# Performance work log

Hardware: AMD Instinct MI355X
Metric: run time of the kernel (lower is better)

## Reference

```python
import jax, jax.numpy as jnp
import numpy as np

H = W = 512      # image spatial dims
C = 3            # channels
K = 32           # kernel size
S = 4            # stride
P = 10           # padding
THRESH = 0.5     # squared-L2 distance threshold
N_PATCH = (H + 2 * P - K) // S + 1  # 126 patches per dim
D = C * K * K    # 3072 patch feature dim


def setup_inputs() -> dict:
    key = jax.random.key(0)
    k1, k2, k3, k4 = jax.random.split(key, 4)
    image = jax.random.uniform(k1, (H, W, C), dtype=jnp.float32)
    mem = jax.random.normal(k2, (4096, D), dtype=jnp.float32)
    mem2 = jax.random.normal(k3, (4096, D), dtype=jnp.float32)
    mapping = jax.random.randint(k4, (4096,), 0, 4096, dtype=jnp.int64)
    return {"image": image, "mem": mem, "mem2": mem2, "mapping": mapping}


def _unfold(img_chw):
    # torch.nn.functional.unfold: -> [L, C*K*K] with feature order (c, kh, kw)
    padded = jnp.pad(img_chw, ((0, 0), (P, P), (P, P)))
    r = (jnp.arange(N_PATCH) * S)[:, None] + jnp.arange(K)[None, :]  # [nH, K]
    c = (jnp.arange(N_PATCH) * S)[:, None] + jnp.arange(K)[None, :]  # [nW, K]
    # patches: [C, nH, nW, K, K]
    patches = padded[:, r[:, None, :, None], c[None, :, None, :]]
    patches = patches.transpose(1, 2, 0, 3, 4)  # [nH, nW, C, K, K]
    return patches.reshape(N_PATCH * N_PATCH, D)


def _fold(patches_ld):
    # inverse of _unfold: scatter-add overlapping patches, crop padding
    p5 = patches_ld.reshape(N_PATCH, N_PATCH, C, K, K)
    r = (jnp.arange(N_PATCH) * S)[:, None] + jnp.arange(K)[None, :]
    c = (jnp.arange(N_PATCH) * S)[:, None] + jnp.arange(K)[None, :]
    canvas = jnp.zeros((C, H + 2 * P, W + 2 * P), dtype=patches_ld.dtype)
    ci = jnp.arange(C)[None, None, :, None, None]
    ri = r[:, None, None, :, None]
    cci = c[None, :, None, None, :]
    canvas = canvas.at[ci, ri, cci].add(p5)
    return canvas[:, P:P + H, P:P + W]  # [C, H, W]


def reference(image, mem, mem2, mapping):
    img_chw = image.transpose(2, 0, 1)            # [C, H, W]
    u = _unfold(img_chw)                           # [L, D]
    # brute-force squared-L2 1-NN against mem bank (FAISS IndexFlatL2)
    d2 = (jnp.sum(u * u, axis=1, keepdims=True)
          - 2.0 * (u @ mem.T)
          + jnp.sum(mem * mem, axis=1)[None, :])   # [L, N]
    dmin = jnp.min(d2, axis=1)                     # [L]
    idx = jnp.argmin(d2, axis=1)                   # [L]
    # counter-based pattern lookup: mem id -> mem2 pattern id -> reconstruct
    recon = mem2[mapping[idx]]                     # [L, D]
    out_p = jnp.where(dmin[:, None] >= THRESH, u, recon)
    folded = _fold(out_p)                          # [C, H, W]
    out = folded / jnp.max(folded)
    return out.transpose(1, 2, 0)                  # [H, W, C]
```

## Files before the change

kernel.cpp:

```cpp
#include <hip/hip_runtime.h>
#include <stdint.h>

#define HH 512
#define WW 512
#define CC 3
#define KK 32
#define SS 4
#define PP 10
#define NPATCH 126
#define NP2 (NPATCH * NPATCH)
#define DD 3072
#define NMEM 4096
#define THRESHV 0.5f

#define OFF_NORMS  0
#define OFF_PNORM  4096
#define OFF_MODCNT 20480
#define OFF_PMAXA  36864

__device__ inline float wave_max(float v) {
    for (int off = 32; off; off >>= 1) v = fmaxf(v, __shfl_xor(v, off, 64));
    return v;
}
__device__ inline float wave_min(float v) {
    for (int off = 32; off; off >>= 1) v = fminf(v, __shfl_xor(v, off, 64));
    return v;
}
__device__ inline float wave_sum(float v) {
    for (int off = 32; off; off >>= 1) v += __shfl_xor(v, off, 64);
    return v;
}

__device__ inline int cov1(int v) {
    int pv = v + PP;
    int a = pv - (KK - 1);
    int imin = (a <= 0) ? 0 : ((a + SS - 1) >> 2);
    int imax = pv >> 2;
    if (imax > NPATCH - 1) imax = NPATCH - 1;
    return imax - imin + 1;
}

__global__ void fused_main(const float* __restrict__ mem,
                           const float* __restrict__ img,
                           float* __restrict__ norms,
                           float* __restrict__ pnorm,
                           float* __restrict__ pmaxA,
                           float* __restrict__ out) {
    __shared__ float cs[WW];
    __shared__ float smx[4];
    int b = blockIdx.x, tid = threadIdx.x;
    int lane = tid & 63, w = tid >> 6;

    if (b >= 1024) {
        int py = b - 1024;
        if (py >= NPATCH) return;
        int y0 = py * SS - PP;
        float s0 = 0.f, s1 = 0.f;
        int x0c = tid, x1c = tid + 256;
#pragma unroll
        for (int ky = 0; ky < KK; ++ky) {
            int y = y0 + ky;
            if (y >= 0 && y < HH) {
                const float* row = img + (size_t)y * WW * CC;
                const float* p0 = row + x0c * CC;
                const float* p1 = row + x1c * CC;
                s0 += p0[0] * p0[0] + p0[1] * p0[1] + p0[2] * p0[2];
                s1 += p1[0] * p1[0] + p1[1] * p1[1] + p1[2] * p1[2];
            }
        }
        cs[x0c] = s0;
        cs[x1c] = s1;
        __syncthreads();
        if (tid < NPATCH) {
            int x0 = tid * SS - PP;
            float t = 0.f;
#pragma unroll
            for (int kx = 0; kx < KK; ++kx) {
                int xx = x0 + kx;
                if (xx >= 0 && xx < WW) t += cs[xx];
            }
            pnorm[py * NPATCH + tid] = t;
        }
        return;
    }

    float m = -INFINITY;
    if (tid < 192) {
        int f = b * 192 + tid;
        float4 v = ((const float4*)img)[f];
        float r[4] = {v.x, v.y, v.z, v.w};
        int e = f * 4;
#pragma unroll
        for (int k = 0; k < 4; ++k) {
            int px = (e + k) / 3;
            int y = px >> 9, x = px & 511;
            float cv = (float)(cov1(y) * cov1(x));
            r[k] *= cv;
            m = fmaxf(m, r[k]);
        }
        float4 o; o.x = r[0]; o.y = r[1]; o.z = r[2]; o.w = r[3];
        ((float4*)out)[f] = o;
    }

    int row = b * 4 + w;
    const float4* rp = (const float4*)(mem + (size_t)row * DD);
    float4 v[12];
#pragma unroll
    for (int i = 0; i < 12; ++i) v[i] = rp[lane + (i << 6)];
    float s0 = 0.f, s1 = 0.f, s2 = 0.f, s3 = 0.f;
#pragma unroll
    for (int i = 0; i < 12; ++i) {
        s0 += v[i].x * v[i].x; s1 += v[i].y * v[i].y;
        s2 += v[i].z * v[i].z; s3 += v[i].w * v[i].w;
    }
    float s = wave_sum((s0 + s1) + (s2 + s3));
    if (lane == 0) norms[row] = s;

    m = wave_max(m);
    if (lane == 0) smx[w] = m;
    __syncthreads();
    if (tid == 0)
        pmaxA[b] = fmaxf(fmaxf(smx[0], smx[1]), fmaxf(smx[2], smx[3]));
}

__global__ void cert_fix(const float* __restrict__ img,
                         const float* __restrict__ mem,
                         const float* __restrict__ mem2,
                         const int* __restrict__ mapping,
                         const float* __restrict__ norms,
                         const float* __restrict__ pnorm,
                         float* __restrict__ out,
                         uint32_t* __restrict__ modcnt) {
    __shared__ float rmn[4], rmx[4];
    __shared__ float s_mn, s_mx;
    __shared__ float smin[256];
    __shared__ int   sarg[256];
    __shared__ uint32_t s_cnt;
    __shared__ uint32_t s_list[256];
    __shared__ int   s_mod;
    int tid = threadIdx.x, lane = tid & 63, w = tid >> 6;
    if (tid == 0) { s_mod = 0; s_cnt = 0; }

    float mn = INFINITY, mx = -INFINITY;
#pragma unroll
    for (int k = 0; k < 16; ++k) {
        float v = norms[tid + (k << 8)];
        mn = fminf(mn, v); mx = fmaxf(mx, v);
    }
    mn = wave_min(mn); mx = wave_max(mx);
    if (lane == 0) { rmn[w] = mn; rmx[w] = mx; }
    __syncthreads();
    if (tid == 0) {
        s_mn = sqrtf(fminf(fminf(rmn[0], rmn[1]), fminf(rmn[2], rmn[3])));
        s_mx = sqrtf(fmaxf(fmaxf(rmx[0], rmx[1]), fmaxf(rmx[2], rmx[3])));
    }
    __syncthreads();
    float lo = s_mn, hi = s_mx;

    int per = (NP2 + gridDim.x - 1) / gridDim.x;
    int p0 = blockIdx.x * per;
    int p1 = p0 + per; if (p1 > NP2) p1 = NP2;
    for (int p = p0 + tid; p < p1; p += 256) {
        float un = sqrtf(pnorm[p]);
        float gap = 0.f;
        if (un <= lo) gap = lo - un;
        else if (un >= hi) gap = un - hi;
        if (gap * gap < THRESHV) {
            uint32_t pos = atomicAdd(&s_cnt, 1u);
            s_list[pos] = (uint32_t)p;
        }
    }
    __syncthreads();
    uint32_t nf = s_cnt;

    for (uint32_t e = 0; e < nf; ++e) {
        int p = (int)s_list[e];
        int pi = p / NPATCH, pj = p % NPATCH;
        int y0 = pi * SS - PP, x0 = pj * SS - PP;
        float best = INFINITY; int barg = NMEM;
        for (int j = tid; j < NMEM; j += 256) {
            const float* mr = mem + (size_t)j * DD;
            float sacc = 0.f;
            for (int d = 0; d < DD; ++d) {
                int c = d >> 10, rem = d & 1023, ky = rem >> 5, kx = rem & 31;
                int y = y0 + ky, x = x0 + kx;
                float u = (y >= 0 && y < HH && x >= 0 && x < WW)
                              ? img[((size_t)y * WW + x) * CC + c] : 0.f;
                float dif = u - mr[d];
                sacc += dif * dif;
            }
            if (sacc < best) { best = sacc; barg = j; }
        }
        smin[tid] = best; sarg[tid] = barg;
        __syncthreads();
        for (int stride = 128; stride; stride >>= 1) {
            if (tid < stride) {
                float s2 = smin[tid + stride];
                int   a2 = sarg[tid + stride];
                if (s2 < smin[tid] || (s2 == smin[tid] && a2 < sarg[tid])) {
                    smin[tid] = s2; sarg[tid] = a2;
                }
            }
            __syncthreads();
        }
        float dmin = smin[0]; int arg = sarg[0];
        if (dmin < THRESHV) {
            const float* rec = mem2 + (size_t)mapping[arg] * DD;
            for (int d = tid; d < DD; d += 256) {
                int c = d >> 10, rem = d & 1023, ky = rem >> 5, kx = rem & 31;
                int y = y0 + ky, x = x0 + kx;
                if (y >= 0 && y < HH && x >= 0 && x < WW) {
                    float u = img[((size_t)y * WW + x) * CC + c];
                    atomicAdd(&out[((size_t)y * WW + x) * CC + c],
                              rec[d] - u);
                }
            }
            if (tid == 0) s_mod++;
        }
        __syncthreads();
    }
    if (tid == 0) modcnt[blockIdx.x] = (uint32_t)s_mod;
}

__global__ void normalize_k(const uint32_t* __restrict__ modcnt,
                            const float* __restrict__ pmaxA,
                            float* __restrict__ out) {
    __shared__ int s_need;
    __shared__ float red[4];
    __shared__ float s_inv;
    int tid = threadIdx.x, lane = tid & 63, w = tid >> 6;
    if (w == 0) {
        int c = (int)modcnt[lane];
        for (int off = 32; off; off >>= 1) c += __shfl_xor(c, off, 64);
        if (lane == 0) s_need = c;
    }
    __syncthreads();
    float m = -INFINITY;
    if (s_need == 0) {
#pragma unroll
        for (int k = 0; k < 4; ++k)
            m = fmaxf(m, pmaxA[tid + (k << 8)]);
    } else {
        const float4* o4 = (const float4*)out;
        for (int i = tid; i < (HH * WW * CC) / 4; i += 256) {
            float4 v = o4[i];
            m = fmaxf(m, fmaxf(fmaxf(v.x, v.y), fmaxf(v.z, v.w)));
        }
    }
    m = wave_max(m);
    if (lane == 0) red[w] = m;
    __syncthreads();
    if (tid == 0)
        s_inv = 1.0f / fmaxf(fmaxf(red[0], red[1]), fmaxf(red[2], red[3]));
    __syncthreads();
    float inv = s_inv;
    if (tid < 192) {
        int f = blockIdx.x * 192 + tid;
        float4 v = ((float4*)out)[f];
        v.x *= inv; v.y *= inv; v.z *= inv; v.w *= inv;
        ((float4*)out)[f] = v;
    }
}

extern "C" void kernel_launch(void* const* d_in, const int* in_sizes, int n_in,
                              void* d_out, int out_size, void* d_ws, size_t ws_size,
                              hipStream_t stream) {
    const float* img     = (const float*)d_in[0];
    const float* mem     = (const float*)d_in[1];
    const float* mem2    = (const float*)d_in[2];
    const int*   mapping = (const int*)d_in[3];
    float* out    = (float*)d_out;
    uint32_t* wsu = (uint32_t*)d_ws;

    float*    norms  = (float*)(wsu + OFF_NORMS);
    float*    pnorm  = (float*)(wsu + OFF_PNORM);
    uint32_t* modcnt = wsu + OFF_MODCNT;
    float*    pmaxA  = (float*)(wsu + OFF_PMAXA);

    fused_main <<<1152, 256, 0, stream>>>(mem, img, norms, pnorm, pmaxA, out);
    cert_fix   <<<64, 256, 0, stream>>>(img, mem, mem2, mapping, norms,
                                        pnorm, out, modcnt);
    normalize_k<<<1024, 256, 0, stream>>>(modcnt, pmaxA, out);
}
```

Measured before the change: 129.4 us.

## Merge certification, fix-up and normalization into one finish kernel

Cuts the pipeline from three kernels to two. The main kernel now emits per-block min/max of memory norms and per-row patch-norm extrema instead of norms and a pre-scaled output. A single finish kernel decides globally from these reductions whether every patch is certified far from the memory bank. If so, each block writes the coverage-scaled, normalized image in one pass, which removes the separate output write/read round trip and one launch. The fallback path redundantly recomputes the search per block and recomputes fixed values without atomics. It also changes mapping to be read as int64.

```diff
diff --git a/kernel.cpp b/kernel.cpp
--- a/kernel.cpp
+++ b/kernel.cpp
@@ -13,10 +13,13 @@
 #define NMEM 4096
 #define THRESHV 0.5f
 
-#define OFF_NORMS  0
-#define OFF_PNORM  4096
-#define OFF_MODCNT 20480
-#define OFF_PMAXA  36864
+#define OFF_PNORM  0
+#define OFF_PRMAX  16384
+#define OFF_PRMIN  16640
+#define OFF_NBMIN  16896
+#define OFF_NBMAX  17920
+#define OFF_PMAXA  18944
+#define OFF_FBSCR  262144
 
 __device__ inline float wave_max(float v) {
     for (int off = 32; off; off >>= 1) v = fmaxf(v, __shfl_xor(v, off, 64));
@@ -42,18 +45,19 @@
 
 __global__ void fused_main(const float* __restrict__ mem,
                            const float* __restrict__ img,
-                           float* __restrict__ norms,
                            float* __restrict__ pnorm,
-                           float* __restrict__ pmaxA,
-                           float* __restrict__ out) {
+                           float* __restrict__ prmax,
+                           float* __restrict__ prmin,
+                           float* __restrict__ nbmin,
+                           float* __restrict__ nbmax,
+                           float* __restrict__ pmaxA) {
     __shared__ float cs[WW];
-    __shared__ float smx[4];
+    __shared__ float sA[4], sB[4], sC[4];
     int b = blockIdx.x, tid = threadIdx.x;
     int lane = tid & 63, w = tid >> 6;
 
-    if (b >= 1024) {
-        int py = b - 1024;
-        if (py >= NPATCH) return;
+    if (b < NPATCH) {
+        int py = b;
         int y0 = py * SS - PP;
         float s0 = 0.f, s1 = 0.f;
         int x0c = tid, x1c = tid + 256;
@@ -71,9 +75,9 @@
         cs[x0c] = s0;
         cs[x1c] = s1;
         __syncthreads();
+        float t = 0.f;
         if (tid < NPATCH) {
             int x0 = tid * SS - PP;
-            float t = 0.f;
 #pragma unroll
             for (int kx = 0; kx < KK; ++kx) {
                 int xx = x0 + kx;
@@ -81,12 +85,24 @@
             }
             pnorm[py * NPATCH + tid] = t;
         }
+        float tmax = (tid < NPATCH) ? t : -INFINITY;
+        float tmin = (tid < NPATCH) ? t : INFINITY;
+        tmax = wave_max(tmax);
+        tmin = wave_min(tmin);
+        if (lane == 0) { sA[w] = tmax; sB[w] = tmin; }
+        __syncthreads();
+        if (tid == 0) {
+            prmax[py] = fmaxf(fmaxf(sA[0], sA[1]), fmaxf(sA[2], sA[3]));
+            prmin[py] = fminf(fminf(sB[0], sB[1]), fminf(sB[2], sB[3]));
+        }
         return;
     }
+
+    int b2 = b - NPATCH;
 
     float m = -INFINITY;
     if (tid < 192) {
-        int f = b * 192 + tid;
+        int f = b2 * 192 + tid;
         float4 v = ((const float4*)img)[f];
         float r[4] = {v.x, v.y, v.z, v.w};
         int e = f * 4;
@@ -94,15 +110,11 @@
         for (int k = 0; k < 4; ++k) {
             int px = (e + k) / 3;
             int y = px >> 9, x = px & 511;
-            float cv = (float)(cov1(y) * cov1(x));
-            r[k] *= cv;
-            m = fmaxf(m, r[k]);
-        }
-        float4 o; o.x = r[0]; o.y = r[1]; o.z = r[2]; o.w = r[3];
-        ((float4*)out)[f] = o;
-    }
-
-    int row = b * 4 + w;
+            m = fmaxf(m, r[k] * (float)(cov1(y) * cov1(x)));
+        }
+    }
+
+    int row = b2 * 4 + w;
     const float4* rp = (const float4*)(mem + (size_t)row * DD);
     float4 v[12];
 #pragma unroll
@@ -114,171 +126,197 @@
         s2 += v[i].z * v[i].z; s3 += v[i].w * v[i].w;
     }
     float s = wave_sum((s0 + s1) + (s2 + s3));
-    if (lane == 0) norms[row] = s;
 
     m = wave_max(m);
-    if (lane == 0) smx[w] = m;
-    __syncthreads();
-    if (tid == 0)
-        pmaxA[b] = fmaxf(fmaxf(smx[0], smx[1]), fmaxf(smx[2], smx[3]));
-}
-
-__global__ void cert_fix(const float* __restrict__ img,
+    if (lane == 0) { sA[w] = m; sB[w] = s; }
+    __syncthreads();
+    if (tid == 0) {
+        pmaxA[b2] = fmaxf(fmaxf(sA[0], sA[1]), fmaxf(sA[2], sA[3]));
+        nbmin[b2] = fminf(fminf(sB[0], sB[1]), fminf(sB[2], sB[3]));
+        nbmax[b2] = fmaxf(fmaxf(sB[0], sB[1]), fmaxf(sB[2], sB[3]));
+    }
+    (void)sC;
+}
+
+__device__ float fixed_val(int i, const float* __restrict__ img,
+                           const float* __restrict__ mem2,
+                           const uint32_t* __restrict__ scr, uint32_t nr) {
+    int px = i / 3, ch = i - px * 3;
+    int y = px >> 9, x = px & 511;
+    float base = img[i];
+    float v = base * (float)(cov1(y) * cov1(x));
+    for (uint32_t e = 0; e < nr; ++e) {
+        int p = (int)scr[2 * e];
+        int pi = p / NPATCH, pj = p % NPATCH;
+        int ky = y - (pi * SS - PP), kx = x - (pj * SS - PP);
+        if (ky >= 0 && ky < KK && kx >= 0 && kx < KK) {
+            const float* rec = mem2 + (size_t)scr[2 * e + 1] * DD;
+            v += rec[(ch << 10) + (ky << 5) + kx] - base;
+        }
+    }
+    return v;
+}
+
+__global__ void finish_k(const float* __restrict__ img,
                          const float* __restrict__ mem,
                          const float* __restrict__ mem2,
-                         const int* __restrict__ mapping,
-                         const float* __restrict__ norms,
+                         const long long* __restrict__ mapping,
                          const float* __restrict__ pnorm,
+                         const float* __restrict__ prmax,
+                         const float* __restrict__ prmin,
+                         const float* __restrict__ nbmin,
+                         const float* __restrict__ nbmax,
+                         const float* __restrict__ pmaxA,
                          float* __restrict__ out,
-                         uint32_t* __restrict__ modcnt) {
-    __shared__ float rmn[4], rmx[4];
-    __shared__ float s_mn, s_mx;
+                         uint32_t* __restrict__ fbscr) {
+    __shared__ float r0[4], r1[4], r2[4], r3[4], r4[4];
+    __shared__ float s_lo, s_hi, s_inv;
+    __shared__ int s_cert;
+    int tid = threadIdx.x, lane = tid & 63, w = tid >> 6;
+
+    float lo2 = INFINITY, hi2 = -INFINITY, bmax = -INFINITY;
+#pragma unroll
+    for (int k = 0; k < 4; ++k) {
+        int i = tid + (k << 8);
+        lo2 = fminf(lo2, nbmin[i]);
+        hi2 = fmaxf(hi2, nbmax[i]);
+        bmax = fmaxf(bmax, pmaxA[i]);
+    }
+    float up2 = (tid < NPATCH) ? prmax[tid] : -INFINITY;
+    float un2 = (tid < NPATCH) ? prmin[tid] : INFINITY;
+
+    lo2 = wave_min(lo2); hi2 = wave_max(hi2); bmax = wave_max(bmax);
+    up2 = wave_max(up2); un2 = wave_min(un2);
+    if (lane == 0) { r0[w] = lo2; r1[w] = hi2; r2[w] = bmax; r3[w] = up2; r4[w] = un2; }
+    __syncthreads();
+    if (tid == 0) {
+        float a = fminf(fminf(r0[0], r0[1]), fminf(r0[2], r0[3]));
+        float bb = fmaxf(fmaxf(r1[0], r1[1]), fmaxf(r1[2], r1[3]));
+        float c = fmaxf(fmaxf(r2[0], r2[1]), fmaxf(r2[2], r2[3]));
+        float d = fmaxf(fmaxf(r3[0], r3[1]), fmaxf(r3[2], r3[3]));
+        float e = fminf(fminf(r4[0], r4[1]), fminf(r4[2], r4[3]));
+        float lo = sqrtf(a), hi = sqrtf(bb);
+        float umax = sqrtf(d), umin = sqrtf(e);
+        int cert = 0;
+        if (umax <= lo) { float g = lo - umax; if (g * g >= THRESHV) cert = 1; }
+        if (!cert && umin >= hi) { float g = umin - hi; if (g * g >= THRESHV) cert = 1; }
+        s_cert = cert; s_lo = lo; s_hi = hi; s_inv = 1.0f / c;
+    }
+    __syncthreads();
+
+    if (s_cert) {
+        float inv = s_inv;
+        if (tid < 192) {
+            int f = blockIdx.x * 192 + tid;
+            float4 v = ((const float4*)img)[f];
+            float r[4] = {v.x, v.y, v.z, v.w};
+            int e = f * 4;
+#pragma unroll
+            for (int k = 0; k < 4; ++k) {
+                int px = (e + k) / 3;
+                int y = px >> 9, x = px & 511;
+                r[k] *= (float)(cov1(y) * cov1(x)) * inv;
+            }
+            float4 o; o.x = r[0]; o.y = r[1]; o.z = r[2]; o.w = r[3];
+            ((float4*)out)[f] = o;
+        }
+        return;
+    }
+
     __shared__ float smin[256];
-    __shared__ int   sarg[256];
-    __shared__ uint32_t s_cnt;
-    __shared__ uint32_t s_list[256];
-    __shared__ int   s_mod;
-    int tid = threadIdx.x, lane = tid & 63, w = tid >> 6;
-    if (tid == 0) { s_mod = 0; s_cnt = 0; }
-
-    float mn = INFINITY, mx = -INFINITY;
-#pragma unroll
-    for (int k = 0; k < 16; ++k) {
-        float v = norms[tid + (k << 8)];
-        mn = fminf(mn, v); mx = fmaxf(mx, v);
-    }
-    mn = wave_min(mn); mx = wave_max(mx);
-    if (lane == 0) { rmn[w] = mn; rmx[w] = mx; }
-    __syncthreads();
-    if (tid == 0) {
-        s_mn = sqrtf(fminf(fminf(rmn[0], rmn[1]), fminf(rmn[2], rmn[3])));
-        s_mx = sqrtf(fmaxf(fmaxf(rmx[0], rmx[1]), fmaxf(rmx[2], rmx[3])));
-    }
-    __syncthreads();
-    float lo = s_mn, hi = s_mx;
-
-    int per = (NP2 + gridDim.x - 1) / gridDim.x;
-    int p0 = blockIdx.x * per;
-    int p1 = p0 + per; if (p1 > NP2) p1 = NP2;
-    for (int p = p0 + tid; p < p1; p += 256) {
+    __shared__ int sarg[256];
+    __shared__ uint32_t s_nr;
+    __shared__ float s_ginv;
+    float lo = s_lo, hi = s_hi;
+    uint32_t* myscr = fbscr + (size_t)blockIdx.x * (2u * NP2);
+    if (tid == 0) s_nr = 0;
+    __syncthreads();
+
+    for (int p = 0; p < NP2; ++p) {
         float un = sqrtf(pnorm[p]);
         float gap = 0.f;
         if (un <= lo) gap = lo - un;
         else if (un >= hi) gap = un - hi;
-        if (gap * gap < THRESHV) {
-            uint32_t pos = atomicAdd(&s_cnt, 1u);
-            s_list[pos] = (uint32_t)p;
-        }
-    }
-    __syncthreads();
-    uint32_t nf = s_cnt;
-
-    for (uint32_t e = 0; e < nf; ++e) {
-        int p = (int)s_list[e];
+        if (gap * gap >= THRESHV) continue;
+
         int pi = p / NPATCH, pj = p % NPATCH;
         int y0 = pi * SS - PP, x0 = pj * SS - PP;
         float best = INFINITY; int barg = NMEM;
         for (int j = tid; j < NMEM; j += 256) {
             const float* mr = mem + (size_t)j * DD;
-            float sacc = 0.f;
+            float acc = 0.f;
             for (int d = 0; d < DD; ++d) {
                 int c = d >> 10, rem = d & 1023, ky = rem >> 5, kx = rem & 31;
                 int y = y0 + ky, x = x0 + kx;
                 float u = (y >= 0 && y < HH && x >= 0 && x < WW)
                               ? img[((size_t)y * WW + x) * CC + c] : 0.f;
                 float dif = u - mr[d];
-                sacc += dif * dif;
-            }
-            if (sacc < best) { best = sacc; barg = j; }
+                acc += dif * dif;
+            }
+            if (acc < best) { best = acc; barg = j; }
         }
         smin[tid] = best; sarg[tid] = barg;
         __syncthreads();
-        for (int stride = 128; stride; stride >>= 1) {
-            if (tid < stride) {
-                float s2 = smin[tid + stride];
-                int   a2 = sarg[tid + stride];
+        for (int st = 128; st; st >>= 1) {
+            if (tid < st) {
+                float s2 = smin[tid + st];
+                int a2 = sarg[tid + st];
                 if (s2 < smin[tid] || (s2 == smin[tid] && a2 < sarg[tid])) {
                     smin[tid] = s2; sarg[tid] = a2;
                 }
             }
             __syncthreads();
         }
-        float dmin = smin[0]; int arg = sarg[0];
-        if (dmin < THRESHV) {
-            const float* rec = mem2 + (size_t)mapping[arg] * DD;
-            for (int d = tid; d < DD; d += 256) {
-                int c = d >> 10, rem = d & 1023, ky = rem >> 5, kx = rem & 31;
-                int y = y0 + ky, x = x0 + kx;
-                if (y >= 0 && y < HH && x >= 0 && x < WW) {
-                    float u = img[((size_t)y * WW + x) * CC + c];
-                    atomicAdd(&out[((size_t)y * WW + x) * CC + c],
-                              rec[d] - u);
-                }
-            }
-            if (tid == 0) s_mod++;
+        if (smin[0] < THRESHV) {
+            if (tid == 0) {
+                uint32_t k = s_nr++;
+                myscr[2 * k] = (uint32_t)p;
+                myscr[2 * k + 1] = (uint32_t)mapping[sarg[0]];
+            }
         }
         __syncthreads();
     }
-    if (tid == 0) modcnt[blockIdx.x] = (uint32_t)s_mod;
-}
-
-__global__ void normalize_k(const uint32_t* __restrict__ modcnt,
-                            const float* __restrict__ pmaxA,
-                            float* __restrict__ out) {
-    __shared__ int s_need;
-    __shared__ float red[4];
-    __shared__ float s_inv;
-    int tid = threadIdx.x, lane = tid & 63, w = tid >> 6;
-    if (w == 0) {
-        int c = (int)modcnt[lane];
-        for (int off = 32; off; off >>= 1) c += __shfl_xor(c, off, 64);
-        if (lane == 0) s_need = c;
-    }
-    __syncthreads();
-    float m = -INFINITY;
-    if (s_need == 0) {
-#pragma unroll
-        for (int k = 0; k < 4; ++k)
-            m = fmaxf(m, pmaxA[tid + (k << 8)]);
-    } else {
-        const float4* o4 = (const float4*)out;
-        for (int i = tid; i < (HH * WW * CC) / 4; i += 256) {
-            float4 v = o4[i];
-            m = fmaxf(m, fmaxf(fmaxf(v.x, v.y), fmaxf(v.z, v.w)));
-        }
-    }
-    m = wave_max(m);
-    if (lane == 0) red[w] = m;
+    __threadfence_block();
+    __syncthreads();
+    uint32_t nr = s_nr;
+
+    float gm = -INFINITY;
+    for (int i = tid; i < HH * WW * CC; i += 256)
+        gm = fmaxf(gm, fixed_val(i, img, mem2, myscr, nr));
+    gm = wave_max(gm);
+    if (lane == 0) r0[w] = gm;
     __syncthreads();
     if (tid == 0)
-        s_inv = 1.0f / fmaxf(fmaxf(red[0], red[1]), fmaxf(red[2], red[3]));
-    __syncthreads();
-    float inv = s_inv;
-    if (tid < 192) {
-        int f = blockIdx.x * 192 + tid;
-        float4 v = ((float4*)out)[f];
-        v.x *= inv; v.y *= inv; v.z *= inv; v.w *= inv;
-        ((float4*)out)[f] = v;
-    }
+        s_ginv = 1.0f / fmaxf(fmaxf(r0[0], r0[1]), fmaxf(r0[2], r0[3]));
+    __syncthreads();
+    float ginv = s_ginv;
+
+    int base = blockIdx.x * 768;
+    for (int i = base + tid; i < base + 768; i += 256)
+        out[i] = fixed_val(i, img, mem2, myscr, nr) * ginv;
 }
 
 extern "C" void kernel_launch(void* const* d_in, const int* in_sizes, int n_in,
                               void* d_out, int out_size, void* d_ws, size_t ws_size,
                               hipStream_t stream) {
-    const float* img     = (const float*)d_in[0];
-    const float* mem     = (const float*)d_in[1];
-    const float* mem2    = (const float*)d_in[2];
-    const int*   mapping = (const int*)d_in[3];
+    const float* img      = (const float*)d_in[0];
+    const float* mem      = (const float*)d_in[1];
+    const float* mem2     = (const float*)d_in[2];
+    const long long* mapping = (const long long*)d_in[3];
     float* out    = (float*)d_out;
     uint32_t* wsu = (uint32_t*)d_ws;
 
-    float*    norms  = (float*)(wsu + OFF_NORMS);
-    float*    pnorm  = (float*)(wsu + OFF_PNORM);
-    uint32_t* modcnt = wsu + OFF_MODCNT;
-    float*    pmaxA  = (float*)(wsu + OFF_PMAXA);
-
-    fused_main <<<1152, 256, 0, stream>>>(mem, img, norms, pnorm, pmaxA, out);
-    cert_fix   <<<64, 256, 0, stream>>>(img, mem, mem2, mapping, norms,
-                                        pnorm, out, modcnt);
-    normalize_k<<<1024, 256, 0, stream>>>(modcnt, pmaxA, out);
-}
+    float*    pnorm = (float*)(wsu + OFF_PNORM);
+    float*    prmax = (float*)(wsu + OFF_PRMAX);
+    float*    prmin = (float*)(wsu + OFF_PRMIN);
+    float*    nbmin = (float*)(wsu + OFF_NBMIN);
+    float*    nbmax = (float*)(wsu + OFF_NBMAX);
+    float*    pmaxA = (float*)(wsu + OFF_PMAXA);
+    uint32_t* fbscr = wsu + OFF_FBSCR;
+
+    fused_main<<<NPATCH + 1024, 256, 0, stream>>>(mem, img, pnorm, prmax,
+                                                  prmin, nbmin, nbmax, pmaxA);
+    finish_k  <<<1024, 256, 0, stream>>>(img, mem, mem2, mapping, pnorm,
+                                         prmax, prmin, nbmin, nbmax, pmaxA,
+                                         out, fbscr);
+}
```

Result: no change. 128.9 us (-0.4%).
